# Kernel optimization log

Measured on AMD Instinct MI355X. Metric: run time of the kernel, lower is better.

## Reference

```python
import jax, jax.numpy as jnp
import numpy as np
from jax import lax

NUM_LAYERS = 2
H = 1024   # per-direction hidden = state_size / 2
IN = 768   # BERT hidden size == input_size
SEQ = 1024


def _init_params(key):
    ks = jax.random.split(key, 4 * NUM_LAYERS * 2)
    mk = lambda k, shape: jax.random.normal(k, shape, jnp.float32) * 0.02
    out = {}
    i = 0
    for d in ("fw", "bw"):
        for l in range(NUM_LAYERS):
            ins = IN if l == 0 else H
            out[f"{d}{l}_Wih"] = mk(ks[i], (4 * H, ins)); i += 1
            out[f"{d}{l}_Whh"] = mk(ks[i], (4 * H, H)); i += 1
            out[f"{d}{l}_bih"] = mk(ks[i], (4 * H,)); i += 1
            out[f"{d}{l}_bhh"] = mk(ks[i], (4 * H,)); i += 1
    return out


def setup_inputs() -> dict:
    key = jax.random.key(0)
    kx, kp = jax.random.split(key)
    inp = {"last_hidden": jax.random.normal(kx, (1, SEQ, IN), jnp.float32)}
    inp.update(_init_params(kp))
    return inp


def _run_direction(x, params):
    """x: [S, in_dim]; params: list of (Wih, Whh, bih, bhh) per layer.
    Stacked LSTMCells (torch gate order i,f,g,o), dropout_amount=0."""
    def step(carry, xt):
        new = []
        inp = xt
        for (h, c), (Wih, Whh, bih, bhh) in zip(carry, params):
            gates = Wih @ inp + bih + Whh @ h + bhh  # [4H]
            i, f, g, o = jnp.split(gates, 4)
            c = jax.nn.sigmoid(f) * c + jax.nn.sigmoid(i) * jnp.tanh(g)
            h = jax.nn.sigmoid(o) * jnp.tanh(c)
            new.append((h, c))
            inp = h
        return tuple(new), inp  # output = top layer h
    init = tuple((jnp.zeros((H,), x.dtype), jnp.zeros((H,), x.dtype)) for _ in params)
    final, outs = lax.scan(step, init, x)
    cs = jnp.stack([c for (_, c) in final])  # [L, H] final cell states
    hs = jnp.stack([h for (h, _) in final])  # [L, H] final hidden states
    return cs, hs, outs                      # outs: [S, H]


def reference(last_hidden, fw0_Wih, fw0_Whh, fw0_bih, fw0_bhh,
              fw1_Wih, fw1_Whh, fw1_bih, fw1_bhh,
              bw0_Wih, bw0_Whh, bw0_bih, bw0_bhh,
              bw1_Wih, bw1_Whh, bw1_bih, bw1_bhh):
    x = last_hidden[0]  # squeeze batch of 1 -> [S, IN]
    fw = [(fw0_Wih, fw0_Whh, fw0_bih, fw0_bhh), (fw1_Wih, fw1_Whh, fw1_bih, fw1_bhh)]
    bw = [(bw0_Wih, bw0_Whh, bw0_bih, bw0_bhh), (bw1_Wih, bw1_Whh, bw1_bih, bw1_bhh)]
    f_c, f_h, f_out = _run_direction(x, fw)
    b_c, b_h, b_out = _run_direction(x[::-1], bw)
    b_out = b_out[::-1]  # re-align backward outputs with token order
    cell_memories = jnp.concatenate([f_c, b_c], axis=1)      # [L, 2H]
    hidden_states = jnp.concatenate([f_h, b_h], axis=1)      # [L, 2H]
    final_outputs = jnp.concatenate([f_out, b_out], axis=1)  # [S, 2H]
    return cell_memories, hidden_states, final_outputs
```

## Files before the change

### kernel.cpp

```cpp
#include <hip/hip_runtime.h>

typedef unsigned int u32;
typedef unsigned short u16;
typedef unsigned long long u64;
typedef __attribute__((ext_vector_type(8))) short v8s;
typedef __attribute__((ext_vector_type(4))) float v4f;

#define VALIDMASK 0x0001000100010001ULL

__device__ __forceinline__ float bf2f(u16 v) { return __uint_as_float(((u32)v) << 16); }
__device__ __forceinline__ u16 f2bf(float f) {
    u32 u = __float_as_uint(f);
    return (u16)((u + 0x7fffu + ((u >> 16) & 1u)) >> 16);
}
__device__ __forceinline__ u32 f2bfo(float f) { return (__float_as_uint(f) >> 16) | 1u; }
__device__ __forceinline__ float sigf(float x) { return 1.0f / (1.0f + __expf(-x)); }
__device__ __forceinline__ float tanhfast(float x) {
    float e = __expf(2.0f * x);
    return 1.0f - 2.0f / (e + 1.0f);
}
__device__ __forceinline__ v8s pack8(v4f a, v4f b) {
    v8s r;
    r[0] = (short)f2bf(a[0]); r[1] = (short)f2bf(a[1]);
    r[2] = (short)f2bf(a[2]); r[3] = (short)f2bf(a[3]);
    r[4] = (short)f2bf(b[0]); r[5] = (short)f2bf(b[1]);
    r[6] = (short)f2bf(b[2]); r[7] = (short)f2bf(b[3]);
    return r;
}

__global__ __launch_bounds__(256) void gemm_ih(
    const float* __restrict__ A, const float* __restrict__ W,
    const float* __restrict__ bih, const float* __restrict__ bhh,
    u16* __restrict__ out, int K)
{
    __shared__ u16 As[128][40];
    __shared__ u16 Bs[128][40];
    const int tm = blockIdx.x, tn = blockIdx.y;
    const int tid = threadIdx.x;
    const int lane = tid & 63;
    const int wv = tid >> 6;
    const int wm = wv >> 1, wn = wv & 1;
    const int fr = lane & 15, fq = lane >> 4;

    v4f acc[4][4] = {};

    for (int kt = 0; kt < K; kt += 32) {
#pragma unroll
        for (int it = 0; it < 2; ++it) {
            int q = tid + it * 256;
            int r = q >> 2;
            int c8 = (q & 3) * 8;
            const float* pa = &A[(size_t)(tm * 128 + r) * K + kt + c8];
            const float* pw = &W[(size_t)(tn * 128 + r) * K + kt + c8];
            *(v8s*)&As[r][c8] = pack8(*(const v4f*)pa, *(const v4f*)(pa + 4));
            *(v8s*)&Bs[r][c8] = pack8(*(const v4f*)pw, *(const v4f*)(pw + 4));
        }
        __syncthreads();
        v8s af[4], bfr[4];
#pragma unroll
        for (int mi = 0; mi < 4; ++mi)
            af[mi] = *(const v8s*)&As[wm * 64 + mi * 16 + fr][fq * 8];
#pragma unroll
        for (int ni = 0; ni < 4; ++ni)
            bfr[ni] = *(const v8s*)&Bs[wn * 64 + ni * 16 + fr][fq * 8];
#pragma unroll
        for (int mi = 0; mi < 4; ++mi)
#pragma unroll
            for (int ni = 0; ni < 4; ++ni)
                acc[mi][ni] = __builtin_amdgcn_mfma_f32_16x16x32_bf16(af[mi], bfr[ni], acc[mi][ni], 0, 0, 0);
        __syncthreads();
    }

#pragma unroll
    for (int ni = 0; ni < 4; ++ni) {
        int col = tn * 128 + wn * 64 + ni * 16 + fr;
        float bias = bih[col] + bhh[col];
#pragma unroll
        for (int mi = 0; mi < 4; ++mi)
#pragma unroll
            for (int j = 0; j < 4; ++j) {
                int row = tm * 128 + wm * 64 + mi * 16 + fq * 4 + j;
                out[(size_t)row * 4096 + col] = f2bf(acc[mi][ni][j] + bias);
            }
    }
}

__global__ __launch_bounds__(64, 1) void lstm_fused(
    const float* __restrict__ fw0_Whh, const float* __restrict__ bw0_Whh,
    const float* __restrict__ fw1_Whh, const float* __restrict__ bw1_Whh,
    const float* __restrict__ fw1_Wih, const float* __restrict__ bw1_Wih,
    const float* __restrict__ fw1_bih, const float* __restrict__ fw1_bhh,
    const float* __restrict__ bw1_bih, const float* __restrict__ bw1_bhh,
    const u16*  __restrict__ precomp0,
    u64* htag0,
    u64* htag1,
    float* __restrict__ out)
{
    extern __shared__ char smem[];
    char* hA = smem + 65536;
    char* hB = smem + 65536 + 2048;
    float* gd = (float*)(smem + 65536 + 4096);

    const int lane = threadIdx.x;
    const int bid = blockIdx.x;
    const int role = bid >> 8;
    const int sub = bid & 255;
    const int d = sub >> 7;
    const int wg = sub & 127;
    const int e0 = wg << 3;
    const int q16 = (lane >> 4) << 4;

    const float* __restrict__ Whh =
        role ? (d ? bw1_Whh : fw1_Whh) : (d ? bw0_Whh : fw0_Whh);

    v8s awf0[32], awf1[32];
    {
        int r0 = lane & 15, r1 = r0 + 16;
        int kq = (lane >> 4) << 3;
        const float* p0 = &Whh[(size_t)((r0 >> 3) * 1024 + e0 + (r0 & 7)) * 1024 + kq];
        const float* p1 = &Whh[(size_t)((r1 >> 3) * 1024 + e0 + (r1 & 7)) * 1024 + kq];
#pragma unroll
        for (int c = 0; c < 32; ++c) {
            awf0[c] = pack8(*(const v4f*)(p0 + 32 * c), *(const v4f*)(p0 + 32 * c + 4));
            awf1[c] = pack8(*(const v4f*)(p1 + 32 * c), *(const v4f*)(p1 + 32 * c + 4));
        }
    }

    float bias_i = 0.f, bias_f = 0.f, bias_g = 0.f, bias_o = 0.f;
    if (role) {
        const float* __restrict__ Wih = d ? bw1_Wih : fw1_Wih;
        for (int i = 0; i < 32; ++i) {
            const float* prow = &Wih[(size_t)((i >> 3) * 1024 + e0 + (i & 7)) * 1024];
            int base = ((lane & 3) << 9) + ((i >> 4) << 8) + ((i & 15) << 4);
            const float* p0 = prow + lane * 8;
            const float* p1 = prow + 512 + lane * 8;
            *(v8s*)(smem + ((lane >> 2) << 11) + base) =
                pack8(*(const v4f*)p0, *(const v4f*)(p0 + 4));
            *(v8s*)(smem + ((16 + (lane >> 2)) << 11) + base) =
                pack8(*(const v4f*)p1, *(const v4f*)(p1 + 4));
        }
        if (lane < 8) {
            const float* bi = d ? bw1_bih : fw1_bih;
            const float* bh = d ? bw1_bhh : fw1_bhh;
            bias_i = bi[e0 + lane]        + bh[e0 + lane];
            bias_f = bi[1024 + e0 + lane] + bh[1024 + e0 + lane];
            bias_g = bi[2048 + e0 + lane] + bh[2048 + e0 + lane];
            bias_o = bi[3072 + e0 + lane] + bh[3072 + e0 + lane];
        }
    }

    u64* hown = (role ? htag1 : htag0) + (size_t)d * 1024 * 256;
    u64* hin  = htag0 + (size_t)d * 1024 * 256;
    float* cm_out = out + role * 2048;
    float* hs_out = out + 4096 + role * 2048;
    float* seq_out = out + 8192;

    float c_state = 0.0f;
    v4f wacc0 = {0.f,0.f,0.f,0.f}, wacc1 = {0.f,0.f,0.f,0.f};
    const int fb = ((lane >> 4) << 9) + ((lane & 15) << 4);

    if (role) {
        u64* p = hin + lane;
        u64 a, b, c2, d2;
        for (;;) {
            a  = __hip_atomic_load(&p[0],   __ATOMIC_RELAXED, __HIP_MEMORY_SCOPE_AGENT);
            b  = __hip_atomic_load(&p[64],  __ATOMIC_RELAXED, __HIP_MEMORY_SCOPE_AGENT);
            c2 = __hip_atomic_load(&p[128], __ATOMIC_RELAXED, __HIP_MEMORY_SCOPE_AGENT);
            d2 = __hip_atomic_load(&p[192], __ATOMIC_RELAXED, __HIP_MEMORY_SCOPE_AGENT);
            if ((((a & b) & (c2 & d2)) & VALIDMASK) == VALIDMASK) break;
            __builtin_amdgcn_s_sleep(1);
        }
        *(u64*)(hB + (lane << 3))        = a;
        *(u64*)(hB + (lane << 3) + 512)  = b;
        *(u64*)(hB + (lane << 3) + 1024) = c2;
        *(u64*)(hB + (lane << 3) + 1536) = d2;
        asm volatile("s_waitcnt lgkmcnt(0)" ::: "memory");
#pragma unroll
        for (int c = 0; c < 32; c += 2) {
            v8s b0 = *(const v8s*)(hB + (c << 6) + q16);
            v8s b1 = *(const v8s*)(hB + ((c + 1) << 6) + q16);
            v8s a00 = *(const v8s*)(smem + (c << 11) + fb);
            v8s a01 = *(const v8s*)(smem + (c << 11) + fb + 256);
            v8s a10 = *(const v8s*)(smem + ((c + 1) << 11) + fb);
            v8s a11 = *(const v8s*)(smem + ((c + 1) << 11) + fb + 256);
            wacc0 = __builtin_amdgcn_mfma_f32_16x16x32_bf16(a00, b0, wacc0, 0, 0, 0);
            wacc1 = __builtin_amdgcn_mfma_f32_16x16x32_bf16(a01, b0, wacc1, 0, 0, 0);
            wacc0 = __builtin_amdgcn_mfma_f32_16x16x32_bf16(a10, b1, wacc0, 0, 0, 0);
            wacc1 = __builtin_amdgcn_mfma_f32_16x16x32_bf16(a11, b1, wacc1, 0, 0, 0);
        }
    }

    for (int s = 0; s < 1024; ++s) {
        v4f acc0a = {0.f,0.f,0.f,0.f}, acc0b = {0.f,0.f,0.f,0.f};
        v4f acc1a = {0.f,0.f,0.f,0.f}, acc1b = {0.f,0.f,0.f,0.f};

        u16 ri = 0, rf = 0, rg = 0, ro = 0;
        if (!role && lane < 8) {
            int sx = d ? (1023 - s) : s;
            const u16* pr = precomp0 + ((size_t)d * 1024 + sx) * 4096 + e0 + lane;
            ri = pr[0]; rf = pr[1024]; rg = pr[2048]; ro = pr[3072];
        }

        if (s > 0) {
            u64* p = hown + (size_t)(s - 1) * 256 + lane;
            u64 a, b, c2, d2;
            for (;;) {
                a  = __hip_atomic_load(&p[0],   __ATOMIC_RELAXED, __HIP_MEMORY_SCOPE_AGENT);
                b  = __hip_atomic_load(&p[64],  __ATOMIC_RELAXED, __HIP_MEMORY_SCOPE_AGENT);
                c2 = __hip_atomic_load(&p[128], __ATOMIC_RELAXED, __HIP_MEMORY_SCOPE_AGENT);
                d2 = __hip_atomic_load(&p[192], __ATOMIC_RELAXED, __HIP_MEMORY_SCOPE_AGENT);
                if ((((a & b) & (c2 & d2)) & VALIDMASK) == VALIDMASK) break;
                __builtin_amdgcn_s_sleep(1);
            }
            __builtin_amdgcn_s_setprio(1);
            *(u64*)(hA + (lane << 3))        = a;
            *(u64*)(hA + (lane << 3) + 512)  = b;
            *(u64*)(hA + (lane << 3) + 1024) = c2;
            *(u64*)(hA + (lane << 3) + 1536) = d2;
            asm volatile("s_waitcnt lgkmcnt(0)" ::: "memory");
#pragma unroll
            for (int c = 0; c < 32; c += 2) {
                v8s b0 = *(const v8s*)(hA + (c << 6) + q16);
                v8s b1 = *(const v8s*)(hA + ((c + 1) << 6) + q16);
                acc0a = __builtin_amdgcn_mfma_f32_16x16x32_bf16(awf0[c], b0, acc0a, 0, 0, 0);
                acc1a = __builtin_amdgcn_mfma_f32_16x16x32_bf16(awf1[c], b0, acc1a, 0, 0, 0);
                acc0b = __builtin_amdgcn_mfma_f32_16x16x32_bf16(awf0[c + 1], b1, acc0b, 0, 0, 0);
                acc1b = __builtin_amdgcn_mfma_f32_16x16x32_bf16(awf1[c + 1], b1, acc1b, 0, 0, 0);
            }
            __builtin_amdgcn_s_setprio(0);
        }

        v4f acc0 = acc0a + acc0b + wacc0;
        v4f acc1 = acc1a + acc1b + wacc1;
        if ((lane & 15) == 0) {
            int rbase = (lane >> 4) << 2;
            *(v4f*)&gd[rbase]      = acc0;
            *(v4f*)&gd[16 + rbase] = acc1;
        }
        asm volatile("s_waitcnt lgkmcnt(0)" ::: "memory");

        float h_new = 0.0f;
        if (lane < 8) {
            float Gi = gd[lane]      + (role ? bias_i : bf2f(ri));
            float Gf = gd[8 + lane]  + (role ? bias_f : bf2f(rf));
            float Gg = gd[16 + lane] + (role ? bias_g : bf2f(rg));
            float Go = gd[24 + lane] + (role ? bias_o : bf2f(ro));
            c_state = sigf(Gf) * c_state + sigf(Gi) * tanhfast(Gg);
            h_new = sigf(Go) * tanhfast(c_state);
        }

        u32 w0 = f2bfo(__shfl(h_new, (lane << 2)))     | (f2bfo(__shfl(h_new, (lane << 2) + 1)) << 16);
        u32 w1 = f2bfo(__shfl(h_new, (lane << 2) + 2)) | (f2bfo(__shfl(h_new, (lane << 2) + 3)) << 16);
        if (lane < 2) {
            u64 val = ((u64)w1 << 32) | w0;
            __hip_atomic_store(&hown[(size_t)s * 256 + (e0 >> 2) + lane], val,
                               __ATOMIC_RELAXED, __HIP_MEMORY_SCOPE_AGENT);
        }

        if (lane < 8) {
            if (role) {
                int rrow = d ? (1023 - s) : s;
                seq_out[(size_t)rrow * 2048 + d * 1024 + e0 + lane] = h_new;
            }
            if (s == 1023) {
                cm_out[d * 1024 + e0 + lane] = c_state;
                hs_out[d * 1024 + e0 + lane] = h_new;
            }
        }

        if (role && s < 1023) {
            wacc0 = (v4f){0.f,0.f,0.f,0.f};
            wacc1 = (v4f){0.f,0.f,0.f,0.f};
            u64* p = hin + (size_t)(s + 1) * 256 + lane;
            u64 a, b, c2, d2;
            for (;;) {
                a  = __hip_atomic_load(&p[0],   __ATOMIC_RELAXED, __HIP_MEMORY_SCOPE_AGENT);
                b  = __hip_atomic_load(&p[64],  __ATOMIC_RELAXED, __HIP_MEMORY_SCOPE_AGENT);
                c2 = __hip_atomic_load(&p[128], __ATOMIC_RELAXED, __HIP_MEMORY_SCOPE_AGENT);
                d2 = __hip_atomic_load(&p[192], __ATOMIC_RELAXED, __HIP_MEMORY_SCOPE_AGENT);
                if ((((a & b) & (c2 & d2)) & VALIDMASK) == VALIDMASK) break;
                __builtin_amdgcn_s_sleep(1);
            }
            *(u64*)(hB + (lane << 3))        = a;
            *(u64*)(hB + (lane << 3) + 512)  = b;
            *(u64*)(hB + (lane << 3) + 1024) = c2;
            *(u64*)(hB + (lane << 3) + 1536) = d2;
            asm volatile("s_waitcnt lgkmcnt(0)" ::: "memory");
#pragma unroll
            for (int c = 0; c < 32; c += 2) {
                v8s b0 = *(const v8s*)(hB + (c << 6) + q16);
                v8s b1 = *(const v8s*)(hB + ((c + 1) << 6) + q16);
                v8s a00 = *(const v8s*)(smem + (c << 11) + fb);
                v8s a01 = *(const v8s*)(smem + (c << 11) + fb + 256);
                v8s a10 = *(const v8s*)(smem + ((c + 1) << 11) + fb);
                v8s a11 = *(const v8s*)(smem + ((c + 1) << 11) + fb + 256);
                wacc0 = __builtin_amdgcn_mfma_f32_16x16x32_bf16(a00, b0, wacc0, 0, 0, 0);
                wacc1 = __builtin_amdgcn_mfma_f32_16x16x32_bf16(a01, b0, wacc1, 0, 0, 0);
                wacc0 = __builtin_amdgcn_mfma_f32_16x16x32_bf16(a10, b1, wacc0, 0, 0, 0);
                wacc1 = __builtin_amdgcn_mfma_f32_16x16x32_bf16(a11, b1, wacc1, 0, 0, 0);
            }
        }
    }
}

extern "C" void kernel_launch(void* const* d_in, const int* in_sizes, int n_in,
                              void* d_out, int out_size, void* d_ws, size_t ws_size,
                              hipStream_t stream) {
    (void)in_sizes; (void)n_in; (void)out_size; (void)ws_size;

    const float* x       = (const float*)d_in[0];
    const float* fw0_Wih = (const float*)d_in[1];
    const float* fw0_Whh = (const float*)d_in[2];
    const float* fw0_bih = (const float*)d_in[3];
    const float* fw0_bhh = (const float*)d_in[4];
    const float* fw1_Wih = (const float*)d_in[5];
    const float* fw1_Whh = (const float*)d_in[6];
    const float* fw1_bih = (const float*)d_in[7];
    const float* fw1_bhh = (const float*)d_in[8];
    const float* bw0_Wih = (const float*)d_in[9];
    const float* bw0_Whh = (const float*)d_in[10];
    const float* bw0_bih = (const float*)d_in[11];
    const float* bw0_bhh = (const float*)d_in[12];
    const float* bw1_Wih = (const float*)d_in[13];
    const float* bw1_Whh = (const float*)d_in[14];
    const float* bw1_bih = (const float*)d_in[15];
    const float* bw1_bhh = (const float*)d_in[16];

    char* ws = (char*)d_ws;
    u16* precomp = (u16*)ws;
    u64* htag0   = (u64*)(ws + (16 << 20));
    u64* htag1   = (u64*)(ws + (20 << 20));
    float* out   = (float*)d_out;

    hipMemsetAsync(htag0, 0, (size_t)8 << 20, stream);

    dim3 g(8, 32);
    gemm_ih<<<g, 256, 0, stream>>>(x, fw0_Wih, fw0_bih, fw0_bhh, precomp, 768);
    gemm_ih<<<g, 256, 0, stream>>>(x, bw0_Wih, bw0_bih, bw0_bhh,
                                   precomp + (size_t)1024 * 4096, 768);

    lstm_fused<<<512, 64, 69760, stream>>>(
        fw0_Whh, bw0_Whh, fw1_Whh, bw1_Whh, fw1_Wih, bw1_Wih,
        fw1_bih, fw1_bhh, bw1_bih, bw1_bhh,
        precomp, htag0, htag1, out);
}
```

Before: 3.222 ms.

## Merge two wavefronts per workgroup to share hidden-state polling and LDS staging

Each workgroup now holds two wavefronts covering 16 hidden units, which halves the grid to 256 blocks. The two waves split the polling of the previous step's hidden-state tags (two u64 per thread instead of four) and share the staged vector in LDS through __syncthreads. The h buffers are double-buffered by step parity so a wave can run ahead without overwriting data the other wave still reads. The aim is to cut per-step global polling latency and traffic. In exchange, the larger LDS footprint (about 136 KB) and an intra-block barrier every step couple the two waves' progress.

```diff
diff --git a/kernel.cpp b/kernel.cpp
--- a/kernel.cpp
+++ b/kernel.cpp
@@ -85,7 +85,7 @@
     }
 }
 
-__global__ __launch_bounds__(64, 1) void lstm_fused(
+__global__ __launch_bounds__(128, 1) void lstm_fused(
     const float* __restrict__ fw0_Whh, const float* __restrict__ bw0_Whh,
     const float* __restrict__ fw1_Whh, const float* __restrict__ bw1_Whh,
     const float* __restrict__ fw1_Wih, const float* __restrict__ bw1_Wih,
@@ -97,18 +97,21 @@
     float* __restrict__ out)
 {
     extern __shared__ char smem[];
-    char* hA = smem + 65536;
-    char* hB = smem + 65536 + 2048;
-    float* gd = (float*)(smem + 65536 + 4096);
-
-    const int lane = threadIdx.x;
+    char* hA0 = smem + 131072;
+    char* hB0 = smem + 131072 + 4096;
+
+    const int tid = threadIdx.x;
+    const int lane = tid & 63;
+    const int w = tid >> 6;
     const int bid = blockIdx.x;
-    const int role = bid >> 8;
-    const int sub = bid & 255;
-    const int d = sub >> 7;
-    const int wg = sub & 127;
-    const int e0 = wg << 3;
+    const int role = bid >> 7;
+    const int d = (bid >> 6) & 1;
+    const int wg = bid & 63;
+    const int e0 = wg << 4;
+    const int ew0 = e0 + (w << 3);
     const int q16 = (lane >> 4) << 4;
+    float* gdw = (float*)(smem + 139264 + (w << 7));
+    char* wih_base = smem + (w << 16);
 
     const float* __restrict__ Whh =
         role ? (d ? bw1_Whh : fw1_Whh) : (d ? bw0_Whh : fw0_Whh);
@@ -117,8 +120,8 @@
     {
         int r0 = lane & 15, r1 = r0 + 16;
         int kq = (lane >> 4) << 3;
-        const float* p0 = &Whh[(size_t)((r0 >> 3) * 1024 + e0 + (r0 & 7)) * 1024 + kq];
-        const float* p1 = &Whh[(size_t)((r1 >> 3) * 1024 + e0 + (r1 & 7)) * 1024 + kq];
+        const float* p0 = &Whh[(size_t)((r0 >> 3) * 1024 + ew0 + (r0 & 7)) * 1024 + kq];
+        const float* p1 = &Whh[(size_t)((r1 >> 3) * 1024 + ew0 + (r1 & 7)) * 1024 + kq];
 #pragma unroll
         for (int c = 0; c < 32; ++c) {
             awf0[c] = pack8(*(const v4f*)(p0 + 32 * c), *(const v4f*)(p0 + 32 * c + 4));
@@ -130,22 +133,22 @@
     if (role) {
         const float* __restrict__ Wih = d ? bw1_Wih : fw1_Wih;
         for (int i = 0; i < 32; ++i) {
-            const float* prow = &Wih[(size_t)((i >> 3) * 1024 + e0 + (i & 7)) * 1024];
+            const float* prow = &Wih[(size_t)((i >> 3) * 1024 + ew0 + (i & 7)) * 1024];
             int base = ((lane & 3) << 9) + ((i >> 4) << 8) + ((i & 15) << 4);
             const float* p0 = prow + lane * 8;
             const float* p1 = prow + 512 + lane * 8;
-            *(v8s*)(smem + ((lane >> 2) << 11) + base) =
+            *(v8s*)(wih_base + ((lane >> 2) << 11) + base) =
                 pack8(*(const v4f*)p0, *(const v4f*)(p0 + 4));
-            *(v8s*)(smem + ((16 + (lane >> 2)) << 11) + base) =
+            *(v8s*)(wih_base + ((16 + (lane >> 2)) << 11) + base) =
                 pack8(*(const v4f*)p1, *(const v4f*)(p1 + 4));
         }
         if (lane < 8) {
             const float* bi = d ? bw1_bih : fw1_bih;
             const float* bh = d ? bw1_bhh : fw1_bhh;
-            bias_i = bi[e0 + lane]        + bh[e0 + lane];
-            bias_f = bi[1024 + e0 + lane] + bh[1024 + e0 + lane];
-            bias_g = bi[2048 + e0 + lane] + bh[2048 + e0 + lane];
-            bias_o = bi[3072 + e0 + lane] + bh[3072 + e0 + lane];
+            bias_i = bi[ew0 + lane]        + bh[ew0 + lane];
+            bias_f = bi[1024 + ew0 + lane] + bh[1024 + ew0 + lane];
+            bias_g = bi[2048 + ew0 + lane] + bh[2048 + ew0 + lane];
+            bias_o = bi[3072 + ew0 + lane] + bh[3072 + ew0 + lane];
         }
     }
 
@@ -160,29 +163,25 @@
     const int fb = ((lane >> 4) << 9) + ((lane & 15) << 4);
 
     if (role) {
-        u64* p = hin + lane;
-        u64 a, b, c2, d2;
+        u64* p = hin + (tid << 1);
+        u64 a, b;
         for (;;) {
-            a  = __hip_atomic_load(&p[0],   __ATOMIC_RELAXED, __HIP_MEMORY_SCOPE_AGENT);
-            b  = __hip_atomic_load(&p[64],  __ATOMIC_RELAXED, __HIP_MEMORY_SCOPE_AGENT);
-            c2 = __hip_atomic_load(&p[128], __ATOMIC_RELAXED, __HIP_MEMORY_SCOPE_AGENT);
-            d2 = __hip_atomic_load(&p[192], __ATOMIC_RELAXED, __HIP_MEMORY_SCOPE_AGENT);
-            if ((((a & b) & (c2 & d2)) & VALIDMASK) == VALIDMASK) break;
+            a = __hip_atomic_load(&p[0], __ATOMIC_RELAXED, __HIP_MEMORY_SCOPE_AGENT);
+            b = __hip_atomic_load(&p[1], __ATOMIC_RELAXED, __HIP_MEMORY_SCOPE_AGENT);
+            if (((a & b) & VALIDMASK) == VALIDMASK) break;
             __builtin_amdgcn_s_sleep(1);
         }
-        *(u64*)(hB + (lane << 3))        = a;
-        *(u64*)(hB + (lane << 3) + 512)  = b;
-        *(u64*)(hB + (lane << 3) + 1024) = c2;
-        *(u64*)(hB + (lane << 3) + 1536) = d2;
-        asm volatile("s_waitcnt lgkmcnt(0)" ::: "memory");
+        *(u64*)(hB0 + (tid << 4))     = a;
+        *(u64*)(hB0 + (tid << 4) + 8) = b;
+        __syncthreads();
 #pragma unroll
         for (int c = 0; c < 32; c += 2) {
-            v8s b0 = *(const v8s*)(hB + (c << 6) + q16);
-            v8s b1 = *(const v8s*)(hB + ((c + 1) << 6) + q16);
-            v8s a00 = *(const v8s*)(smem + (c << 11) + fb);
-            v8s a01 = *(const v8s*)(smem + (c << 11) + fb + 256);
-            v8s a10 = *(const v8s*)(smem + ((c + 1) << 11) + fb);
-            v8s a11 = *(const v8s*)(smem + ((c + 1) << 11) + fb + 256);
+            v8s b0 = *(const v8s*)(hB0 + (c << 6) + q16);
+            v8s b1 = *(const v8s*)(hB0 + ((c + 1) << 6) + q16);
+            v8s a00 = *(const v8s*)(wih_base + (c << 11) + fb);
+            v8s a01 = *(const v8s*)(wih_base + (c << 11) + fb + 256);
+            v8s a10 = *(const v8s*)(wih_base + ((c + 1) << 11) + fb);
+            v8s a11 = *(const v8s*)(wih_base + ((c + 1) << 11) + fb + 256);
             wacc0 = __builtin_amdgcn_mfma_f32_16x16x32_bf16(a00, b0, wacc0, 0, 0, 0);
             wacc1 = __builtin_amdgcn_mfma_f32_16x16x32_bf16(a01, b0, wacc1, 0, 0, 0);
             wacc0 = __builtin_amdgcn_mfma_f32_16x16x32_bf16(a10, b1, wacc0, 0, 0, 0);
@@ -193,35 +192,32 @@
     for (int s = 0; s < 1024; ++s) {
         v4f acc0a = {0.f,0.f,0.f,0.f}, acc0b = {0.f,0.f,0.f,0.f};
         v4f acc1a = {0.f,0.f,0.f,0.f}, acc1b = {0.f,0.f,0.f,0.f};
+        char* Abuf = hA0 + ((s & 1) << 11);
 
         u16 ri = 0, rf = 0, rg = 0, ro = 0;
         if (!role && lane < 8) {
             int sx = d ? (1023 - s) : s;
-            const u16* pr = precomp0 + ((size_t)d * 1024 + sx) * 4096 + e0 + lane;
+            const u16* pr = precomp0 + ((size_t)d * 1024 + sx) * 4096 + ew0 + lane;
             ri = pr[0]; rf = pr[1024]; rg = pr[2048]; ro = pr[3072];
         }
 
         if (s > 0) {
-            u64* p = hown + (size_t)(s - 1) * 256 + lane;
-            u64 a, b, c2, d2;
+            u64* p = hown + (size_t)(s - 1) * 256 + (tid << 1);
+            u64 a, b;
             for (;;) {
-                a  = __hip_atomic_load(&p[0],   __ATOMIC_RELAXED, __HIP_MEMORY_SCOPE_AGENT);
-                b  = __hip_atomic_load(&p[64],  __ATOMIC_RELAXED, __HIP_MEMORY_SCOPE_AGENT);
-                c2 = __hip_atomic_load(&p[128], __ATOMIC_RELAXED, __HIP_MEMORY_SCOPE_AGENT);
-                d2 = __hip_atomic_load(&p[192], __ATOMIC_RELAXED, __HIP_MEMORY_SCOPE_AGENT);
-                if ((((a & b) & (c2 & d2)) & VALIDMASK) == VALIDMASK) break;
+                a = __hip_atomic_load(&p[0], __ATOMIC_RELAXED, __HIP_MEMORY_SCOPE_AGENT);
+                b = __hip_atomic_load(&p[1], __ATOMIC_RELAXED, __HIP_MEMORY_SCOPE_AGENT);
+                if (((a & b) & VALIDMASK) == VALIDMASK) break;
                 __builtin_amdgcn_s_sleep(1);
             }
+            *(u64*)(Abuf + (tid << 4))     = a;
+            *(u64*)(Abuf + (tid << 4) + 8) = b;
+            __syncthreads();
             __builtin_amdgcn_s_setprio(1);
-            *(u64*)(hA + (lane << 3))        = a;
-            *(u64*)(hA + (lane << 3) + 512)  = b;
-            *(u64*)(hA + (lane << 3) + 1024) = c2;
-            *(u64*)(hA + (lane << 3) + 1536) = d2;
-            asm volatile("s_waitcnt lgkmcnt(0)" ::: "memory");
 #pragma unroll
             for (int c = 0; c < 32; c += 2) {
-                v8s b0 = *(const v8s*)(hA + (c << 6) + q16);
-                v8s b1 = *(const v8s*)(hA + ((c + 1) << 6) + q16);
+                v8s b0 = *(const v8s*)(Abuf + (c << 6) + q16);
+                v8s b1 = *(const v8s*)(Abuf + ((c + 1) << 6) + q16);
                 acc0a = __builtin_amdgcn_mfma_f32_16x16x32_bf16(awf0[c], b0, acc0a, 0, 0, 0);
                 acc1a = __builtin_amdgcn_mfma_f32_16x16x32_bf16(awf1[c], b0, acc1a, 0, 0, 0);
                 acc0b = __builtin_amdgcn_mfma_f32_16x16x32_bf16(awf0[c + 1], b1, acc0b, 0, 0, 0);
@@ -234,17 +230,17 @@
         v4f acc1 = acc1a + acc1b + wacc1;
         if ((lane & 15) == 0) {
             int rbase = (lane >> 4) << 2;
-            *(v4f*)&gd[rbase]      = acc0;
-            *(v4f*)&gd[16 + rbase] = acc1;
+            *(v4f*)&gdw[rbase]      = acc0;
+            *(v4f*)&gdw[16 + rbase] = acc1;
         }
         asm volatile("s_waitcnt lgkmcnt(0)" ::: "memory");
 
         float h_new = 0.0f;
         if (lane < 8) {
-            float Gi = gd[lane]      + (role ? bias_i : bf2f(ri));
-            float Gf = gd[8 + lane]  + (role ? bias_f : bf2f(rf));
-            float Gg = gd[16 + lane] + (role ? bias_g : bf2f(rg));
-            float Go = gd[24 + lane] + (role ? bias_o : bf2f(ro));
+            float Gi = gdw[lane]      + (role ? bias_i : bf2f(ri));
+            float Gf = gdw[8 + lane]  + (role ? bias_f : bf2f(rf));
+            float Gg = gdw[16 + lane] + (role ? bias_g : bf2f(rg));
+            float Go = gdw[24 + lane] + (role ? bias_o : bf2f(ro));
             c_state = sigf(Gf) * c_state + sigf(Gi) * tanhfast(Gg);
             h_new = sigf(Go) * tanhfast(c_state);
         }
@@ -253,47 +249,44 @@
         u32 w1 = f2bfo(__shfl(h_new, (lane << 2) + 2)) | (f2bfo(__shfl(h_new, (lane << 2) + 3)) << 16);
         if (lane < 2) {
             u64 val = ((u64)w1 << 32) | w0;
-            __hip_atomic_store(&hown[(size_t)s * 256 + (e0 >> 2) + lane], val,
+            __hip_atomic_store(&hown[(size_t)s * 256 + (e0 >> 2) + (w << 1) + lane], val,
                                __ATOMIC_RELAXED, __HIP_MEMORY_SCOPE_AGENT);
         }
 
         if (lane < 8) {
             if (role) {
                 int rrow = d ? (1023 - s) : s;
-                seq_out[(size_t)rrow * 2048 + d * 1024 + e0 + lane] = h_new;
+                seq_out[(size_t)rrow * 2048 + d * 1024 + ew0 + lane] = h_new;
             }
             if (s == 1023) {
-                cm_out[d * 1024 + e0 + lane] = c_state;
-                hs_out[d * 1024 + e0 + lane] = h_new;
+                cm_out[d * 1024 + ew0 + lane] = c_state;
+                hs_out[d * 1024 + ew0 + lane] = h_new;
             }
         }
 
         if (role && s < 1023) {
             wacc0 = (v4f){0.f,0.f,0.f,0.f};
             wacc1 = (v4f){0.f,0.f,0.f,0.f};
-            u64* p = hin + (size_t)(s + 1) * 256 + lane;
-            u64 a, b, c2, d2;
+            char* Bbuf = hB0 + (((s + 1) & 1) << 11);
+            u64* p = hin + (size_t)(s + 1) * 256 + (tid << 1);
+            u64 a, b;
             for (;;) {
-                a  = __hip_atomic_load(&p[0],   __ATOMIC_RELAXED, __HIP_MEMORY_SCOPE_AGENT);
-                b  = __hip_atomic_load(&p[64],  __ATOMIC_RELAXED, __HIP_MEMORY_SCOPE_AGENT);
-                c2 = __hip_atomic_load(&p[128], __ATOMIC_RELAXED, __HIP_MEMORY_SCOPE_AGENT);
-                d2 = __hip_atomic_load(&p[192], __ATOMIC_RELAXED, __HIP_MEMORY_SCOPE_AGENT);
-                if ((((a & b) & (c2 & d2)) & VALIDMASK) == VALIDMASK) break;
+                a = __hip_atomic_load(&p[0], __ATOMIC_RELAXED, __HIP_MEMORY_SCOPE_AGENT);
+                b = __hip_atomic_load(&p[1], __ATOMIC_RELAXED, __HIP_MEMORY_SCOPE_AGENT);
+                if (((a & b) & VALIDMASK) == VALIDMASK) break;
                 __builtin_amdgcn_s_sleep(1);
             }
-            *(u64*)(hB + (lane << 3))        = a;
-            *(u64*)(hB + (lane << 3) + 512)  = b;
-            *(u64*)(hB + (lane << 3) + 1024) = c2;
-            *(u64*)(hB + (lane << 3) + 1536) = d2;
-            asm volatile("s_waitcnt lgkmcnt(0)" ::: "memory");
+            *(u64*)(Bbuf + (tid << 4))     = a;
+            *(u64*)(Bbuf + (tid << 4) + 8) = b;
+            __syncthreads();
 #pragma unroll
             for (int c = 0; c < 32; c += 2) {
-                v8s b0 = *(const v8s*)(hB + (c << 6) + q16);
-                v8s b1 = *(const v8s*)(hB + ((c + 1) << 6) + q16);
-                v8s a00 = *(const v8s*)(smem + (c << 11) + fb);
-                v8s a01 = *(const v8s*)(smem + (c << 11) + fb + 256);
-                v8s a10 = *(const v8s*)(smem + ((c + 1) << 11) + fb);
-                v8s a11 = *(const v8s*)(smem + ((c + 1) << 11) + fb + 256);
+                v8s b0 = *(const v8s*)(Bbuf + (c << 6) + q16);
+                v8s b1 = *(const v8s*)(Bbuf + ((c + 1) << 6) + q16);
+                v8s a00 = *(const v8s*)(wih_base + (c << 11) + fb);
+                v8s a01 = *(const v8s*)(wih_base + (c << 11) + fb + 256);
+                v8s a10 = *(const v8s*)(wih_base + ((c + 1) << 11) + fb);
+                v8s a11 = *(const v8s*)(wih_base + ((c + 1) << 11) + fb + 256);
                 wacc0 = __builtin_amdgcn_mfma_f32_16x16x32_bf16(a00, b0, wacc0, 0, 0, 0);
                 wacc1 = __builtin_amdgcn_mfma_f32_16x16x32_bf16(a01, b0, wacc1, 0, 0, 0);
                 wacc0 = __builtin_amdgcn_mfma_f32_16x16x32_bf16(a10, b1, wacc0, 0, 0, 0);
@@ -339,7 +332,7 @@
     gemm_ih<<<g, 256, 0, stream>>>(x, bw0_Wih, bw0_bih, bw0_bhh,
                                    precomp + (size_t)1024 * 4096, 768);
 
-    lstm_fused<<<512, 64, 69760, stream>>>(
+    lstm_fused<<<256, 128, 139520, stream>>>(
         fw0_Whh, bw0_Whh, fw1_Whh, bw1_Whh, fw1_Wih, bw1_Wih,
         fw1_bih, fw1_bhh, bw1_bih, bw1_bhh,
         precomp, htag0, htag1, out);
```

Result: slower. 3.910 ms (+21.4%).
